# Kernel optimization log

Measured on AMD Instinct MI355X. Metric: run time of the kernel, lower is better.

## Reference

```python
import jax, jax.numpy as jnp
import numpy as np

EMBED_DIM = 1024
NUM_HEADS = 16
HEAD_DIM = EMBED_DIM // NUM_HEADS


def setup_inputs() -> dict:
    key = jax.random.key(0)
    ks = jax.random.split(key, 11)
    L, N, E = 2048, 2, EMBED_DIM
    S = 2048
    def xavier(k, shape):
        fan_in, fan_out = shape[1], shape[0]
        limit = float(np.sqrt(6.0 / (fan_in + fan_out)))
        return jax.random.uniform(k, shape, jnp.float32, -limit, limit)
    return {
        "query": jax.random.normal(ks[0], (L, N, E), jnp.float32),
        "key": jax.random.normal(ks[1], (S, N, E), jnp.float32),
        "value": jax.random.normal(ks[2], (S, N, E), jnp.float32),
        "Wq": xavier(ks[3], (E, E)), "bq": jnp.zeros((E,), jnp.float32),
        "Wk": xavier(ks[4], (E, E)), "bk": jnp.zeros((E,), jnp.float32),
        "Wv": xavier(ks[5], (E, E)), "bv": jnp.zeros((E,), jnp.float32),
        "Wo": xavier(ks[6], (E, E)), "bo": jnp.zeros((E,), jnp.float32),
    }


def reference(query, key, value, Wq, bq, Wk, bk, Wv, bv, Wo, bo):
    # query/key/value: [L, N, E] (seq-first, batch_first=False)
    L, N, E = query.shape
    S = key.shape[0]
    H, D = NUM_HEADS, HEAD_DIM
    q = query @ Wq.T + bq   # [L, N, E]
    k = key @ Wk.T + bk     # [S, N, E]
    v = value @ Wv.T + bv   # [S, N, E]
    # [L, N*H, D] -> [N*H, L, D]
    q = q.reshape(L, N * H, D).transpose(1, 0, 2)
    k = k.reshape(S, N * H, D).transpose(1, 0, 2)
    v = v.reshape(S, N * H, D).transpose(1, 0, 2)
    scores = jnp.einsum("bld,bsd->bls", q, k) / jnp.sqrt(jnp.float32(D))  # [N*H, L, S]
    attn = jax.nn.softmax(scores, axis=-1)  # dropout p=0.0 -> identity
    out = jnp.einsum("bls,bsd->bld", attn, v)  # [N*H, L, D]
    out = out.transpose(1, 0, 2).reshape(L, N, E)
    attn_output = out @ Wo.T + bo  # [L, N, E]
    # need_weights=True, average_attn_weights=True
    attn_weights = attn.reshape(N, H, L, S).mean(axis=1)  # [N, L, S]
    return attn_output, attn_weights
```

## Files before the change

### kernel.cpp

```cpp
#include <hip/hip_runtime.h>

#define EDIM 1024
#define LSEQ 2048
#define NBATCH 2
#define NHEADS 16
#define HDIM 64
#define QSCALE 0.18033688011112042f

typedef unsigned short us;
typedef __attribute__((ext_vector_type(8))) short short8;
typedef __attribute__((ext_vector_type(4))) float floatx4;
typedef __attribute__((ext_vector_type(16))) float floatx16;

#define MFMA16(a, b, c) __builtin_amdgcn_mfma_f32_16x16x32_bf16((a), (b), (c), 0, 0, 0)
#define MFMA32(a, b, c) __builtin_amdgcn_mfma_f32_32x32x16_bf16((a), (b), (c), 0, 0, 0)
#define ZERO16 ((floatx16){0.f,0.f,0.f,0.f,0.f,0.f,0.f,0.f,0.f,0.f,0.f,0.f,0.f,0.f,0.f,0.f})

__device__ __forceinline__ us f2bf(float f) {
  unsigned int u = __float_as_uint(f);
  u += 0x7fffu + ((u >> 16) & 1u);
  return (us)(u >> 16);
}

__device__ __forceinline__ void gload16(const void* g, void* l) {
  __builtin_amdgcn_global_load_lds((const __attribute__((address_space(1))) unsigned int*)g,
                                   (__attribute__((address_space(3))) unsigned int*)l, 16, 0, 0);
}

__device__ __forceinline__ unsigned int cvtpk(float lo, float hi_) {
  unsigned int r;
  asm("v_cvt_pk_bf16_f32 %0, %1, %2" : "=v"(r) : "v"(lo), "v"(hi_));
  return r;
}
__device__ __forceinline__ void plswap(unsigned int& a, unsigned int& b) {
  asm("v_permlane32_swap_b32 %0, %1" : "+v"(a), "+v"(b));
}
__device__ __forceinline__ short8 mkfrag(unsigned int a, unsigned int b, unsigned int c,
                                         unsigned int d) {
  union { unsigned int u[4]; short8 v; } x;
  x.u[0] = a; x.u[1] = b; x.u[2] = c; x.u[3] = d;
  return x.v;
}
__device__ __forceinline__ void pack2(const floatx16 p, short8& f0, short8& f1) {
  unsigned int A = cvtpk(p[0], p[1]), B = cvtpk(p[4], p[5]); plswap(A, B);
  unsigned int C = cvtpk(p[2], p[3]), D = cvtpk(p[6], p[7]); plswap(C, D);
  f0 = mkfrag(A, C, B, D);
  unsigned int E = cvtpk(p[8], p[9]), F = cvtpk(p[12], p[13]); plswap(E, F);
  unsigned int G = cvtpk(p[10], p[11]), H = cvtpk(p[14], p[15]); plswap(G, H);
  f1 = mkfrag(E, G, F, H);
}

__global__ void k_f2bf_all(const float* q, const float* k, const float* v,
                           const float* wq, const float* wk, const float* wv, const float* wo,
                           us* dq, us* dk, us* dv, us* dwq, us* dwk, us* dwv, us* dwo) {
  const int z = blockIdx.y;
  const float* s; us* d; int n8;
  if (z == 0)      { s = q;  d = dq;  n8 = 524288; }
  else if (z == 1) { s = k;  d = dk;  n8 = 524288; }
  else if (z == 2) { s = v;  d = dv;  n8 = 524288; }
  else if (z == 3) { s = wq; d = dwq; n8 = 131072; }
  else if (z == 4) { s = wk; d = dwk; n8 = 131072; }
  else if (z == 5) { s = wv; d = dwv; n8 = 131072; }
  else             { s = wo; d = dwo; n8 = 131072; }
  int i = blockIdx.x * blockDim.x + threadIdx.x;
  int stride = gridDim.x * blockDim.x;
  for (; i < n8; i += stride) {
    float4 a = ((const float4*)s)[2 * i];
    float4 b = ((const float4*)s)[2 * i + 1];
    union { us u[8]; uint4 vv; } o;
    o.u[0] = f2bf(a.x); o.u[1] = f2bf(a.y); o.u[2] = f2bf(a.z); o.u[3] = f2bf(a.w);
    o.u[4] = f2bf(b.x); o.u[5] = f2bf(b.y); o.u[6] = f2bf(b.z); o.u[7] = f2bf(b.w);
    ((uint4*)d)[i] = o.vv;
  }
}

template <int MODE>
__device__ __forceinline__ void gemm_core(us* pool,
                                          const us* __restrict__ A, const us* __restrict__ B,
                                          const float* __restrict__ bias, void* __restrict__ outp,
                                          int row0, int col0, float scale) {
  us* As = pool;
  us* Bs = pool + 4096;
  const int t = threadIdx.x;
  const int w = t >> 6, lane = t & 63;
  const int g = lane >> 4, lr = lane & 15;
  const int wm = (w & 1) * 64, wn = (w >> 1) * 64;
  const int srow = lane >> 2, scol = (lane & 3) * 8;
  const int cA = 2 * w;
  const us* Asrc = A + (size_t)(row0 + cA * 16 + srow) * EDIM + scol;
  const us* Bsrc = B + (size_t)(col0 + cA * 16 + srow) * EDIM + scol;

  floatx4 acc[4][4];
#pragma unroll
  for (int mi = 0; mi < 4; ++mi)
#pragma unroll
    for (int ni = 0; ni < 4; ++ni) acc[mi][ni] = (floatx4){0.f, 0.f, 0.f, 0.f};

  for (int k0 = 0; k0 < EDIM; k0 += 32) {
    gload16(Asrc + k0, As + cA * 512);
    gload16(Asrc + 16 * EDIM + k0, As + cA * 512 + 512);
    gload16(Bsrc + k0, Bs + cA * 512);
    gload16(Bsrc + 16 * EDIM + k0, Bs + cA * 512 + 512);
    __syncthreads();
    short8 af[4], bfr[4];
#pragma unroll
    for (int mi = 0; mi < 4; ++mi) af[mi] = *(const short8*)&As[(wm + mi * 16 + lr) * 32 + g * 8];
#pragma unroll
    for (int ni = 0; ni < 4; ++ni) bfr[ni] = *(const short8*)&Bs[(wn + ni * 16 + lr) * 32 + g * 8];
#pragma unroll
    for (int mi = 0; mi < 4; ++mi)
#pragma unroll
      for (int ni = 0; ni < 4; ++ni) acc[mi][ni] = MFMA16(af[mi], bfr[ni], acc[mi][ni]);
    __syncthreads();
  }

  if (MODE == 1) {
    us* Ct = pool;
#pragma unroll
    for (int ni = 0; ni < 4; ++ni) {
      const int colloc = wn + ni * 16 + lr;
      const float bv = bias[col0 + colloc];
#pragma unroll
      for (int mi = 0; mi < 4; ++mi) {
        const int b = wm + mi * 16 + 4 * g;
        unsigned int lo = (unsigned int)f2bf(acc[mi][ni][0] + bv) |
                          ((unsigned int)f2bf(acc[mi][ni][2] + bv) << 16);
        unsigned int hi = (unsigned int)f2bf(acc[mi][ni][1] + bv) |
                          ((unsigned int)f2bf(acc[mi][ni][3] + bv) << 16);
        *(unsigned int*)&Ct[colloc * 136 + (b >> 1)] = lo;
        *(unsigned int*)&Ct[colloc * 136 + 64 + (b >> 1)] = hi;
      }
    }
    __syncthreads();
    const int rr = t >> 1, half = t & 1;
    const int c = col0 + rr, h = c >> 6, d = c & 63;
    us* dst = (us*)outp + (((size_t)half * NHEADS + h) * HDIM + d) * LSEQ + (row0 >> 1);
    const us* srcRow = &Ct[rr * 136 + half * 64];
#pragma unroll
    for (int j = 0; j < 8; ++j)
      *(uint4*)(dst + j * 8) = *(const uint4*)(srcRow + j * 8);
  } else {
#pragma unroll
    for (int ni = 0; ni < 4; ++ni) {
      const int col = col0 + wn + ni * 16 + lr;
      const float bv = bias[col];
#pragma unroll
      for (int mi = 0; mi < 4; ++mi) {
#pragma unroll
        for (int i = 0; i < 4; ++i) {
          const int row = row0 + wm + mi * 16 + g * 4 + i;
          const float v = (acc[mi][ni][i] + bv) * scale;
          if (MODE == 2) {
            ((float*)outp)[(size_t)row * EDIM + col] = v;
          } else {
            const int n = row & 1, sq = row >> 1;
            const int h = col >> 6, d = col & 63;
            ((us*)outp)[(((size_t)n * NHEADS + h) * LSEQ + sq) * HDIM + d] = f2bf(v);
          }
        }
      }
    }
  }
}

__global__ __launch_bounds__(256) void k_gemm_qkv(
    const us* __restrict__ Xq, const us* __restrict__ Xk, const us* __restrict__ Xv,
    const us* __restrict__ Wqb, const us* __restrict__ Wkb, const us* __restrict__ Wvb,
    const float* __restrict__ bq, const float* __restrict__ bk, const float* __restrict__ bv,
    us* __restrict__ qo, us* __restrict__ ko, us* __restrict__ vo) {
  __shared__ us pool[17408];
  const int z = blockIdx.z;
  if (z == 0)      gemm_core<0>(pool, Xq, Wqb, bq, qo, blockIdx.x * 128, blockIdx.y * 128, QSCALE);
  else if (z == 1) gemm_core<0>(pool, Xk, Wkb, bk, ko, blockIdx.x * 128, blockIdx.y * 128, 1.0f);
  else             gemm_core<1>(pool, Xv, Wvb, bv, vo, blockIdx.x * 128, blockIdx.y * 128, 1.0f);
}

__global__ __launch_bounds__(256) void k_gemm_o(const us* __restrict__ A, const us* __restrict__ B,
                                                const float* __restrict__ bias, float* __restrict__ out) {
  __shared__ us pool[8192];
  gemm_core<2>(pool, A, B, bias, out, blockIdx.x * 128, blockIdx.y * 128, 1.0f);
}

__global__ __launch_bounds__(256) void k_attn(const us* __restrict__ qb, const us* __restrict__ kb,
                                              const us* __restrict__ vt, float* __restrict__ rell,
                                              us* __restrict__ O) {
  __shared__ us Ks[2][4096];
  __shared__ us Vs[2][4096];
  __shared__ float elt[4][32];
  const int bh = blockIdx.x;
  const int l0 = blockIdx.y * 128;
  const int t = threadIdx.x, w = t >> 6, lane = t & 63;
  const int ql = lane & 31, hi = lane >> 5;

  short8 qf[4];
  {
    const us* qptr = qb + ((size_t)bh * LSEQ + l0 + w * 32 + ql) * HDIM + hi * 8;
#pragma unroll
    for (int dt = 0; dt < 4; ++dt) qf[dt] = *(const short8*)(qptr + dt * 16);
  }

  int off0[4], off1[4];
#pragma unroll
  for (int j = 0; j < 4; ++j) {
    off0[j] = ql * 64 + (((2 * j + hi) ^ (ql & 7)) << 3);
    off1[j] = (32 + ql) * 64 + (((2 * j + hi) ^ (ql & 7)) << 3);
  }

  const int j0 = 2 * w, j1 = 2 * w + 1;
  const int srA = lane >> 3;
  const int scA = ((lane & 7) ^ (lane >> 3)) * 8;
  const us* Kbase = kb + (size_t)bh * LSEQ * HDIM;
  const us* Vbase = vt + (size_t)bh * HDIM * LSEQ;
  const us* Ksrc0 = Kbase + (j0 * 8 + srA) * HDIM + scA;
  const us* Ksrc1 = Kbase + (j1 * 8 + srA) * HDIM + scA;
  const us* Vsrc0 = Vbase + (size_t)(j0 * 8 + srA) * LSEQ + scA;
  const us* Vsrc1 = Vbase + (size_t)(j1 * 8 + srA) * LSEQ + scA;

  floatx16 oacc0 = ZERO16, oacc1 = ZERO16;
  float ellacc = 0.f;

  gload16(Ksrc0, &Ks[0][j0 * 512]); gload16(Ksrc1, &Ks[0][j1 * 512]);
  gload16(Vsrc0, &Vs[0][j0 * 512]); gload16(Vsrc1, &Vs[0][j1 * 512]);
  __syncthreads();

  for (int it = 0; it < 32; ++it) {
    const int cur = it & 1;
    if (it < 31) {
      const int so = (it + 1) * 64;
      us* Kn = Ks[cur ^ 1]; us* Vn = Vs[cur ^ 1];
      gload16(Ksrc0 + so * HDIM, Kn + j0 * 512);
      gload16(Ksrc1 + so * HDIM, Kn + j1 * 512);
      gload16(Vsrc0 + so, Vn + j0 * 512);
      gload16(Vsrc1 + so, Vn + j1 * 512);
    }
    const us* Kc = Ks[cur];
    const us* Vc = Vs[cur];

    floatx16 acc0 = ZERO16, acc1 = ZERO16;
#pragma unroll
    for (int dt = 0; dt < 4; ++dt) {
      acc0 = MFMA32(*(const short8*)&Kc[off0[dt]], qf[dt], acc0);
      acc1 = MFMA32(*(const short8*)&Kc[off1[dt]], qf[dt], acc1);
    }
#pragma unroll
    for (int r = 0; r < 16; ++r) {
      acc0[r] = __builtin_amdgcn_exp2f(acc0[r]); ellacc += acc0[r];
      acc1[r] = __builtin_amdgcn_exp2f(acc1[r]); ellacc += acc1[r];
    }
    short8 pa0, pa1, pa2, pa3;
    pack2(acc0, pa0, pa1);
    pack2(acc1, pa2, pa3);
#pragma unroll
    for (int dt2 = 0; dt2 < 2; ++dt2) {
      floatx16& oa = dt2 ? oacc1 : oacc0;
      const int* off = dt2 ? off1 : off0;
      oa = MFMA32(pa0, *(const short8*)&Vc[off[0]], oa);
      oa = MFMA32(pa1, *(const short8*)&Vc[off[1]], oa);
      oa = MFMA32(pa2, *(const short8*)&Vc[off[2]], oa);
      oa = MFMA32(pa3, *(const short8*)&Vc[off[3]], oa);
    }
    __syncthreads();
  }

  const float elltot = ellacc + __shfl_xor(ellacc, 32);
  if (lane < 32) {
    const float r0 = 1.0f / elltot;
    elt[w][lane] = r0;
    rell[(size_t)bh * LSEQ + l0 + w * 32 + lane] = r0;
  }
  const int n = bh >> 4, hh = bh & 15;
  us* obase = O + (size_t)n * EDIM + (size_t)hh * HDIM;
#pragma unroll
  for (int r = 0; r < 16; ++r) {
    const int q = (r & 3) + 8 * (r >> 2) + 4 * hi;
    const float rl = elt[w][q];
    const size_t l = l0 + w * 32 + q;
    obase[l * (NBATCH * EDIM) + ql] = f2bf(oacc0[r] * rl);
    obase[l * (NBATCH * EDIM) + 32 + ql] = f2bf(oacc1[r] * rl);
  }
}

__global__ __launch_bounds__(256, 2) void k_weights(const us* __restrict__ qb, const us* __restrict__ kb,
                                                    const float* __restrict__ rell,
                                                    float* __restrict__ Wout) {
  __shared__ us Ks[2][4096];
  const int l0 = blockIdx.x * 256;
  const int s0 = blockIdx.y * 64;
  const int n = blockIdx.z;
  const int t = threadIdx.x, w = t >> 6, lane = t & 63;
  const int ql = lane & 31, hi = lane >> 5;
  const int lbase = l0 + w * 64;
  const int j0 = 2 * w, j1 = 2 * w + 1;
  const int srA = lane >> 3;
  const int scA = ((lane & 7) ^ (lane >> 3)) * 8;
  const us* Kb0 = kb + ((size_t)(n * NHEADS) * LSEQ + s0 + j0 * 8 + srA) * HDIM + scA;
  const us* Kb1 = kb + ((size_t)(n * NHEADS) * LSEQ + s0 + j1 * 8 + srA) * HDIM + scA;

  int off0[4], off1[4];
#pragma unroll
  for (int j = 0; j < 4; ++j) {
    off0[j] = ql * 64 + (((2 * j + hi) ^ (ql & 7)) << 3);
    off1[j] = (32 + ql) * 64 + (((2 * j + hi) ^ (ql & 7)) << 3);
  }

  floatx16 wa00 = ZERO16, wa01 = ZERO16, wa10 = ZERO16, wa11 = ZERO16;

  gload16(Kb0, &Ks[0][j0 * 512]); gload16(Kb1, &Ks[0][j1 * 512]);

  short8 qc0[4], qc1[4];
  float rlc0, rlc1;
  {
    const us* qp0 = qb + ((size_t)(n * NHEADS) * LSEQ + lbase + ql) * HDIM + hi * 8;
    const us* qp1 = qp0 + 32 * HDIM;
#pragma unroll
    for (int dt = 0; dt < 4; ++dt) {
      qc0[dt] = *(const short8*)(qp0 + dt * 16);
      qc1[dt] = *(const short8*)(qp1 + dt * 16);
    }
    rlc0 = rell[(size_t)(n * NHEADS) * LSEQ + lbase + ql];
    rlc1 = rell[(size_t)(n * NHEADS) * LSEQ + lbase + 32 + ql];
  }
  __syncthreads();

  for (int h = 0; h < NHEADS; ++h) {
    const int cur = h & 1;
    short8 qn0[4], qn1[4];
    float rln0 = 0.f, rln1 = 0.f;
    if (h < NHEADS - 1) {
      us* Kn2 = Ks[cur ^ 1];
      gload16(Kb0 + (size_t)(h + 1) * LSEQ * HDIM, Kn2 + j0 * 512);
      gload16(Kb1 + (size_t)(h + 1) * LSEQ * HDIM, Kn2 + j1 * 512);
      const us* qp0 = qb + ((size_t)(n * NHEADS + h + 1) * LSEQ + lbase + ql) * HDIM + hi * 8;
      const us* qp1 = qp0 + 32 * HDIM;
#pragma unroll
      for (int dt = 0; dt < 4; ++dt) {
        qn0[dt] = *(const short8*)(qp0 + dt * 16);
        qn1[dt] = *(const short8*)(qp1 + dt * 16);
      }
      rln0 = rell[(size_t)(n * NHEADS + h + 1) * LSEQ + lbase + ql];
      rln1 = rell[(size_t)(n * NHEADS + h + 1) * LSEQ + lbase + 32 + ql];
    }
    const us* Kc = Ks[cur];
    short8 kf0[4], kf1[4];
#pragma unroll
    for (int dt = 0; dt < 4; ++dt) {
      kf0[dt] = *(const short8*)&Kc[off0[dt]];
      kf1[dt] = *(const short8*)&Kc[off1[dt]];
    }
    {
      floatx16 aA = ZERO16, aB = ZERO16;
#pragma unroll
      for (int dt = 0; dt < 4; ++dt) {
        aA = MFMA32(kf0[dt], qc0[dt], aA);
        aB = MFMA32(kf1[dt], qc0[dt], aB);
      }
#pragma unroll
      for (int r = 0; r < 16; ++r) {
        wa00[r] += __builtin_amdgcn_exp2f(aA[r]) * rlc0;
        wa01[r] += __builtin_amdgcn_exp2f(aB[r]) * rlc0;
      }
    }
    {
      floatx16 cA = ZERO16, cB = ZERO16;
#pragma unroll
      for (int dt = 0; dt < 4; ++dt) {
        cA = MFMA32(kf0[dt], qc1[dt], cA);
        cB = MFMA32(kf1[dt], qc1[dt], cB);
      }
#pragma unroll
      for (int r = 0; r < 16; ++r) {
        wa10[r] += __builtin_amdgcn_exp2f(cA[r]) * rlc1;
        wa11[r] += __builtin_amdgcn_exp2f(cB[r]) * rlc1;
      }
    }
#pragma unroll
    for (int dt = 0; dt < 4; ++dt) { qc0[dt] = qn0[dt]; qc1[dt] = qn1[dt]; }
    rlc0 = rln0; rlc1 = rln1;
    __syncthreads();
  }

  float* wb0 = Wout + (size_t)n * LSEQ * LSEQ + (size_t)(lbase + ql) * LSEQ + s0;
  float* wb1 = Wout + (size_t)n * LSEQ * LSEQ + (size_t)(lbase + 32 + ql) * LSEQ + s0;
#pragma unroll
  for (int r = 0; r < 16; ++r) {
    const int cr = (r & 3) + 8 * (r >> 2) + 4 * hi;
    wb0[cr] = wa00[r] * 0.0625f;
    wb0[32 + cr] = wa01[r] * 0.0625f;
    wb1[cr] = wa10[r] * 0.0625f;
    wb1[32 + cr] = wa11[r] * 0.0625f;
  }
}

extern "C" void kernel_launch(void* const* d_in, const int* in_sizes, int n_in,
                              void* d_out, int out_size, void* d_ws, size_t ws_size,
                              hipStream_t stream) {
  const float* query = (const float*)d_in[0];
  const float* key   = (const float*)d_in[1];
  const float* value = (const float*)d_in[2];
  const float* Wq = (const float*)d_in[3]; const float* bq = (const float*)d_in[4];
  const float* Wk = (const float*)d_in[5]; const float* bk = (const float*)d_in[6];
  const float* Wv = (const float*)d_in[7]; const float* bv = (const float*)d_in[8];
  const float* Wo = (const float*)d_in[9]; const float* bo = (const float*)d_in[10];

  const size_t MB = 1u << 20;
  char* ws = (char*)d_ws;
  us* Xq  = (us*)(ws + 0 * MB);
  us* Xk  = (us*)(ws + 8 * MB);
  us* Xv  = (us*)(ws + 16 * MB);
  us* Wqb = (us*)(ws + 24 * MB);
  us* Wkb = (us*)(ws + 26 * MB);
  us* Wvb = (us*)(ws + 28 * MB);
  us* Wob = (us*)(ws + 30 * MB);
  us* qbuf = (us*)(ws + 32 * MB);
  us* kbuf = (us*)(ws + 40 * MB);
  us* Vt   = (us*)(ws + 48 * MB);
  us* Obuf = (us*)(ws + 56 * MB);
  float* rell = (float*)(ws + 64 * MB);

  k_f2bf_all<<<dim3(256, 7), 256, 0, stream>>>(query, key, value, Wq, Wk, Wv, Wo,
                                               Xq, Xk, Xv, Wqb, Wkb, Wvb, Wob);

  k_gemm_qkv<<<dim3(32, 8, 3), 256, 0, stream>>>(Xq, Xk, Xv, Wqb, Wkb, Wvb, bq, bk, bv,
                                                 qbuf, kbuf, Vt);

  k_attn<<<dim3(32, 16), 256, 0, stream>>>(qbuf, kbuf, Vt, rell, Obuf);

  k_gemm_o<<<dim3(32, 8), 256, 0, stream>>>(Obuf, Wob, bo, (float*)d_out);
  k_weights<<<dim3(8, 32, 2), 256, 0, stream>>>(qbuf, kbuf, rell, (float*)d_out + 4194304);
}
```

Before: 173.3 us.

## Double-buffer GEMM shared tiles and raise wave priority around attention MFMAs

The shared GEMM core now keeps two LDS buffers for the A and B tiles. It prefetches the next K-slice while computing the current one, which removes one barrier per iteration and overlaps global loads with MFMA work. The output-projection kernel's shared pool doubles to hold both buffers. The attention loop also wraps its two MFMA phases in s_setprio so matrix work gets issue priority over waves doing exp or loads. The cost is more LDS per block, which can lower occupancy.

```diff
diff --git a/kernel.cpp b/kernel.cpp
--- a/kernel.cpp
+++ b/kernel.cpp
@@ -79,8 +79,8 @@
                                           const us* __restrict__ A, const us* __restrict__ B,
                                           const float* __restrict__ bias, void* __restrict__ outp,
                                           int row0, int col0, float scale) {
-  us* As = pool;
-  us* Bs = pool + 4096;
+  us* const Asb[2] = {pool, pool + 8192};
+  us* const Bsb[2] = {pool + 4096, pool + 12288};
   const int t = threadIdx.x;
   const int w = t >> 6, lane = t & 63;
   const int g = lane >> 4, lr = lane & 15;
@@ -96,17 +96,29 @@
 #pragma unroll
     for (int ni = 0; ni < 4; ++ni) acc[mi][ni] = (floatx4){0.f, 0.f, 0.f, 0.f};
 
+  gload16(Asrc, Asb[0] + cA * 512);
+  gload16(Asrc + 16 * EDIM, Asb[0] + cA * 512 + 512);
+  gload16(Bsrc, Bsb[0] + cA * 512);
+  gload16(Bsrc + 16 * EDIM, Bsb[0] + cA * 512 + 512);
+  __syncthreads();
+
   for (int k0 = 0; k0 < EDIM; k0 += 32) {
-    gload16(Asrc + k0, As + cA * 512);
-    gload16(Asrc + 16 * EDIM + k0, As + cA * 512 + 512);
-    gload16(Bsrc + k0, Bs + cA * 512);
-    gload16(Bsrc + 16 * EDIM + k0, Bs + cA * 512 + 512);
-    __syncthreads();
+    const int cur = (k0 >> 5) & 1;
+    if (k0 + 32 < EDIM) {
+      us* An = Asb[cur ^ 1];
+      us* Bn = Bsb[cur ^ 1];
+      gload16(Asrc + k0 + 32, An + cA * 512);
+      gload16(Asrc + 16 * EDIM + k0 + 32, An + cA * 512 + 512);
+      gload16(Bsrc + k0 + 32, Bn + cA * 512);
+      gload16(Bsrc + 16 * EDIM + k0 + 32, Bn + cA * 512 + 512);
+    }
+    const us* Ac = Asb[cur];
+    const us* Bc = Bsb[cur];
     short8 af[4], bfr[4];
 #pragma unroll
-    for (int mi = 0; mi < 4; ++mi) af[mi] = *(const short8*)&As[(wm + mi * 16 + lr) * 32 + g * 8];
-#pragma unroll
-    for (int ni = 0; ni < 4; ++ni) bfr[ni] = *(const short8*)&Bs[(wn + ni * 16 + lr) * 32 + g * 8];
+    for (int mi = 0; mi < 4; ++mi) af[mi] = *(const short8*)&Ac[(wm + mi * 16 + lr) * 32 + g * 8];
+#pragma unroll
+    for (int ni = 0; ni < 4; ++ni) bfr[ni] = *(const short8*)&Bc[(wn + ni * 16 + lr) * 32 + g * 8];
 #pragma unroll
     for (int mi = 0; mi < 4; ++mi)
 #pragma unroll
@@ -177,7 +189,7 @@
 
 __global__ __launch_bounds__(256) void k_gemm_o(const us* __restrict__ A, const us* __restrict__ B,
                                                 const float* __restrict__ bias, float* __restrict__ out) {
-  __shared__ us pool[8192];
+  __shared__ us pool[16384];
   gemm_core<2>(pool, A, B, bias, out, blockIdx.x * 128, blockIdx.y * 128, 1.0f);
 }
 
@@ -237,11 +249,13 @@
     const us* Vc = Vs[cur];
 
     floatx16 acc0 = ZERO16, acc1 = ZERO16;
+    __builtin_amdgcn_s_setprio(1);
 #pragma unroll
     for (int dt = 0; dt < 4; ++dt) {
       acc0 = MFMA32(*(const short8*)&Kc[off0[dt]], qf[dt], acc0);
       acc1 = MFMA32(*(const short8*)&Kc[off1[dt]], qf[dt], acc1);
     }
+    __builtin_amdgcn_s_setprio(0);
 #pragma unroll
     for (int r = 0; r < 16; ++r) {
       acc0[r] = __builtin_amdgcn_exp2f(acc0[r]); ellacc += acc0[r];
@@ -250,6 +264,7 @@
     short8 pa0, pa1, pa2, pa3;
     pack2(acc0, pa0, pa1);
     pack2(acc1, pa2, pa3);
+    __builtin_amdgcn_s_setprio(1);
 #pragma unroll
     for (int dt2 = 0; dt2 < 2; ++dt2) {
       floatx16& oa = dt2 ? oacc1 : oacc0;
@@ -259,6 +274,7 @@
       oa = MFMA32(pa2, *(const short8*)&Vc[off[2]], oa);
       oa = MFMA32(pa3, *(const short8*)&Vc[off[3]], oa);
     }
+    __builtin_amdgcn_s_setprio(0);
     __syncthreads();
   }
 
```

New measurement: 171.6 us. About the same (-1.0%).
